# Kernel tuning notes

Hardware: AMD Instinct MI355X
Metric: run time of the kernel (lower is better)

## Reference

```python
import jax, jax.numpy as jnp
import numpy as np

B, S, D = 2, 2048, 2048
H = 16
KV_RANK = 512
NOPE, ROPE = 128, 64
QK_HD = NOPE + ROPE  # 192
V_HD = 128
SCALE = QK_HD ** -0.5
EPS = 1.1920929e-07  # torch RMSNorm default eps = finfo(fp32).eps
NEG = -1e9


def rmsnorm(x, w):
    return x * jax.lax.rsqrt(jnp.mean(x * x, axis=-1, keepdims=True) + EPS) * w


def apply_rope(x, freqs):
    # x: (b, s, h, r) interleaved pairs; freqs: (s, r//2) angles
    sh = x.shape
    xr = x.reshape(*sh[:-1], -1, 2)
    a, b = xr[..., 0], xr[..., 1]
    cos = jnp.cos(freqs)[None, :, None, :]
    sin = jnp.sin(freqs)[None, :, None, :]
    return jnp.stack([a * cos - b * sin, a * sin + b * cos], axis=-1).reshape(sh)


def setup_inputs() -> dict:
    key = jax.random.key(0)
    ks = jax.random.split(key, 8)
    inv = lambda k, shape, fan_in: jax.random.uniform(k, shape, jnp.float32, -1.0, 1.0) / np.sqrt(fan_in)
    x = jax.random.normal(ks[0], (B, S, D), jnp.float32)
    freqs = jax.random.uniform(ks[1], (S, ROPE // 2), jnp.float32) * np.float32(np.pi)
    mask = jnp.where(jnp.triu(jnp.ones((S, S), bool), k=1), jnp.float32(NEG), jnp.float32(0.0))
    wq_w = inv(ks[2], (H * QK_HD, D), D)
    wq_b = jnp.zeros((H * QK_HD,), jnp.float32)
    wkv_a_w = inv(ks[3], (KV_RANK + ROPE, D), D)
    wkv_a_b = jnp.zeros((KV_RANK + ROPE,), jnp.float32)
    kv_norm_w = jnp.ones((KV_RANK,), jnp.float32)
    wkv_b_w = inv(ks[4], (H * (NOPE + V_HD), KV_RANK), KV_RANK)
    wo_w = inv(ks[5], (D, H * V_HD), H * V_HD)
    wo_b = jnp.zeros((D,), jnp.float32)
    return dict(x=x, freqs=freqs, mask=mask, wq_w=wq_w, wq_b=wq_b,
                wkv_a_w=wkv_a_w, wkv_a_b=wkv_a_b, kv_norm_w=kv_norm_w,
                wkv_b_w=wkv_b_w, wo_w=wo_w, wo_b=wo_b)


def reference(x, freqs, mask, wq_w, wq_b, wkv_a_w, wkv_a_b, kv_norm_w, wkv_b_w, wo_w, wo_b):
    b, s, _ = x.shape
    # q projection (q_lora_rank == 0 path)
    q = (x @ wq_w.T + wq_b).reshape(b, s, H, QK_HD)
    q_nope, q_pe = q[..., :NOPE], q[..., NOPE:]
    q_pe = apply_rope(q_pe, freqs)
    # latent kv projection
    kv = x @ wkv_a_w.T + wkv_a_b
    kv, k_pe = kv[..., :KV_RANK], kv[..., KV_RANK:]
    k_pe = apply_rope(k_pe[:, :, None, :], freqs)[:, :, 0, :]  # (b, t, r)
    kv_proj = rmsnorm(kv, kv_norm_w)  # (b, t, c)
    wkv_b = wkv_b_w.reshape(H, NOPE + V_HD, KV_RANK)
    # absorb K-nope projection into q
    q_nope = jnp.einsum('bshd,hdc->bshc', q_nope, wkv_b[:, :NOPE])
    scores = (jnp.einsum('bshc,btc->bsht', q_nope, kv_proj)
              + jnp.einsum('bshr,btr->bsht', q_pe, k_pe)) * SCALE
    scores = scores + mask[None, :, None, :]
    scores = jax.nn.softmax(scores.astype(jnp.float32), axis=-1).astype(x.dtype)
    out = jnp.einsum('bsht,btc->bshc', scores, kv_proj)
    out = jnp.einsum('bshc,hdc->bshd', out, wkv_b[:, -V_HD:])
    return out.reshape(b, s, H * V_HD) @ wo_w.T + wo_b
```

## Files before the change

kernel.cpp:

```cpp
#include <hip/hip_runtime.h>
#include <hip/hip_bf16.h>
#include <math.h>

#define B_ 2
#define S_ 2048
#define H_ 16
#define SCALE_ 0.07216878364870323f
#define SL2_ (0.07216878364870323f * 1.4426950408889634f)
#define EPS_ 1.1920929e-07f
#define M0_ 8.0f

typedef __attribute__((ext_vector_type(8))) short bf16x8;
typedef __attribute__((ext_vector_type(4))) float f32x4;
union U4 { uint4 u; bf16x8 v; f32x4 f; };

__device__ __forceinline__ uint bfbits(float x) {
    uint u = __float_as_uint(x);
    return (u + 0x7fffu + ((u >> 16) & 1u)) >> 16;
}
__device__ __forceinline__ uint pack2bf(float a, float b) {
    return bfbits(a) | (bfbits(b) << 16);
}
__device__ __forceinline__ uint cvtpk(float a, float b) {
    uint r;
    asm("v_cvt_pk_bf16_f32 %0, %1, %2" : "=v"(r) : "v"(a), "v"(b));
    return r;
}
__device__ __forceinline__ void gld_lds16(const ushort* g, ushort* l) {
    __builtin_amdgcn_global_load_lds(
        (const __attribute__((address_space(1))) uint*)g,
        (__attribute__((address_space(3))) uint*)l, 16, 0, 0);
}

template<int OM>
__global__ __launch_bounds__(256) void mgemm(
    const ushort* __restrict__ A, int lda, long long aOff1, long long aOff2,
    const ushort* __restrict__ Bm, int ldb, long long bOff1, long long bOff2,
    const float* __restrict__ bias, float scale,
    void* __restrict__ Cv, int ldc, long long cOff1, long long cOff2,
    int K, int zDiv)
{
    __shared__ ushort As[128 * 32];
    __shared__ ushort Bs[128 * 32];

    const int z = blockIdx.z;
    const int z1 = z % zDiv, z2 = z / zDiv;
    A  += z1 * aOff1 + z2 * aOff2;
    Bm += z1 * bOff1 + z2 * bOff2;
    const long long cBase = z1 * cOff1 + z2 * cOff2;

    int bx = blockIdx.x, by = blockIdx.y;
    {
        const int gx = gridDim.x, total = gx * gridDim.y;
        if ((total & 7) == 0) {
            const int flat = bx + gx * by;
            const int nx = total >> 3;
            const int flat2 = (flat & 7) * nx + (flat >> 3);
            bx = flat2 % gx;
            by = flat2 / gx;
        }
    }
    const int n0 = bx * 128;
    const int m0 = by * 128;
    const int tid = threadIdx.x;
    const int w   = tid >> 6;
    const int l   = tid & 63;
    const int m   = l & 15;
    const int q4  = l >> 4;
    const int mw  = (w & 1) * 64;
    const int nw  = (w >> 1) * 64;
    const int sr  = l >> 2;
    const int sc  = l & 3;

    f32x4 acc[4][4];
#pragma unroll
    for (int i = 0; i < 4; ++i)
#pragma unroll
        for (int j = 0; j < 4; ++j) acc[i][j] = (f32x4){0.f, 0.f, 0.f, 0.f};

    for (int k0 = 0; k0 < K; k0 += 32) {
#pragma unroll
        for (int jj = 0; jj < 2; ++jj) {
            const int slot = w * 2 + jj;
            const int row  = slot * 16 + sr;
            const int g    = sc ^ ((row >> 1) & 3);
            gld_lds16(&A[(long long)(m0 + row) * lda + k0 + g * 8], &As[slot * 512]);
            gld_lds16(&Bm[(long long)(n0 + row) * ldb + k0 + g * 8], &Bs[slot * 512]);
        }
        __syncthreads();

        U4 af[4], bf[4];
#pragma unroll
        for (int i = 0; i < 4; ++i) {
            const int ra = mw + i * 16 + m;
            af[i].u = *(const uint4*)&As[ra * 32 + (q4 ^ ((ra >> 1) & 3)) * 8];
            const int rb = nw + i * 16 + m;
            bf[i].u = *(const uint4*)&Bs[rb * 32 + (q4 ^ ((rb >> 1) & 3)) * 8];
        }
#pragma unroll
        for (int i = 0; i < 4; ++i)
#pragma unroll
            for (int j = 0; j < 4; ++j)
                acc[i][j] = __builtin_amdgcn_mfma_f32_16x16x32_bf16(
                    af[i].v, bf[j].v, acc[i][j], 0, 0, 0);
        __syncthreads();
    }

#pragma unroll
    for (int j = 0; j < 4; ++j) {
        const int cn = n0 + nw + j * 16 + m;
        const float bv = bias ? bias[cn] : 0.0f;
#pragma unroll
        for (int i = 0; i < 4; ++i) {
            const int rw = m0 + mw + i * 16 + q4 * 4;
#pragma unroll
            for (int r = 0; r < 4; ++r) {
                const float val = acc[i][j][r] * scale + bv;
                if (OM == 0) {
                    ((float*)Cv)[cBase + (long long)(rw + r) * ldc + cn] = val;
                } else if (OM == 2) {
                    const int t = rw + r, d = cn;
                    const long long idx =
                        ((((long long)(z2 * 64 + (t >> 5)) * 16 + z1) * 8
                          + (d >> 5) * 2 + ((t >> 4) & 1)) * 64
                         + ((d >> 3) & 3) * 16 + (t & 15)) * 8 + (d & 7);
                    ((ushort*)Cv)[idx] = (ushort)bfbits(val);
                } else {
                    const int d = rw + r, t = cn;
                    const long long idx =
                        ((((long long)(z2 * 64 + (t >> 5)) * 16 + z1) * 8
                          + (d >> 4)) * 64
                         + ((t >> 3) & 3) * 16 + (d & 15)) * 8 + (t & 7);
                    ((ushort*)Cv)[idx] = (ushort)bfbits(val);
                }
            }
        }
    }
}

__global__ __launch_bounds__(256) void conv_all(
    const float* __restrict__ x, const float* __restrict__ wq,
    const float* __restrict__ wkva, const float* __restrict__ wo,
    const float* __restrict__ wkvb,
    ushort* __restrict__ x_bf, ushort* __restrict__ wq_bf,
    ushort* __restrict__ wkva_bf, ushort* __restrict__ wo_bf,
    ushort* __restrict__ wkvbK, ushort* __restrict__ wkvbV)
{
    const int bid = blockIdx.x;
    const int tid = threadIdx.x;
    if (bid < 8192) {
        const long long i = ((long long)bid * 256 + tid) * 4;
        float4 v = *(const float4*)&x[i];
        uint2 p; p.x = pack2bf(v.x, v.y); p.y = pack2bf(v.z, v.w);
        *(uint2*)&x_bf[i] = p;
    } else if (bid < 14336) {
        const long long i = ((long long)(bid - 8192) * 256 + tid) * 4;
        float4 v = *(const float4*)&wq[i];
        uint2 p; p.x = pack2bf(v.x, v.y); p.y = pack2bf(v.z, v.w);
        *(uint2*)&wq_bf[i] = p;
    } else if (bid < 15616) {
        const int i = ((bid - 14336) * 256 + tid) * 4;
        const int r = i >> 11;
        uint2 p = make_uint2(0u, 0u);
        if (r < 576) {
            float4 v = *(const float4*)&wkva[i];
            p.x = pack2bf(v.x, v.y); p.y = pack2bf(v.z, v.w);
        }
        *(uint2*)&wkva_bf[i] = p;
    } else if (bid < 19712) {
        const long long i = ((long long)(bid - 15616) * 256 + tid) * 4;
        float4 v = *(const float4*)&wo[i];
        uint2 p; p.x = pack2bf(v.x, v.y); p.y = pack2bf(v.z, v.w);
        *(uint2*)&wo_bf[i] = p;
    } else if (bid < 20736) {
        const int i = ((bid - 19712) * 256 + tid) * 4;
        const int h = i >> 16, rem = i & 65535;
        float4 v = *(const float4*)&wkvb[((long long)(h * 256)) * 512 + rem];
        uint2 p; p.x = pack2bf(v.x, v.y); p.y = pack2bf(v.z, v.w);
        *(uint2*)&wkvbK[i] = p;
    } else {
        const int i = ((bid - 20736) * 256 + tid) * 4;
        const int h = i >> 16, rem = i & 65535;
        float4 v = *(const float4*)&wkvb[((long long)(h * 256 + 128)) * 512 + rem];
        uint2 p; p.x = pack2bf(v.x, v.y); p.y = pack2bf(v.z, v.w);
        *(uint2*)&wkvbV[i] = p;
    }
}

__global__ __launch_bounds__(256) void qprep(
    const float* __restrict__ q_raw, const float* __restrict__ freqs,
    ushort* __restrict__ q192)
{
    const int idx = blockIdx.x * 256 + threadIdx.x;
    const int row = idx / 48;
    const int c4  = idx % 48;
    const int bs = row >> 4, h = row & 15;
    const float* src = q_raw + (long long)bs * 3072 + h * 192;
    if (c4 < 32) {
        const int d = c4 * 4;
        float4 v = *(const float4*)&src[d];
        uint2 p;
        p.x = pack2bf(v.x * SL2_, v.y * SL2_);
        p.y = pack2bf(v.z * SL2_, v.w * SL2_);
        *(uint2*)&q192[(long long)row * 192 + d] = p;
    } else {
        const int j = c4 - 32;
        const int s = bs & 2047;
        const float f0 = freqs[s * 32 + j * 2];
        const float f1 = freqs[s * 32 + j * 2 + 1];
        float c0, s0, c1, s1;
        __sincosf(f0, &s0, &c0);
        __sincosf(f1, &s1, &c1);
        float4 v = *(const float4*)&src[128 + j * 4];
        uint2 p;
        p.x = pack2bf((v.x * c0 - v.y * s0) * SL2_, (v.x * s0 + v.y * c0) * SL2_);
        p.y = pack2bf((v.z * c1 - v.w * s1) * SL2_, (v.z * s1 + v.w * c1) * SL2_);
        *(uint2*)&q192[(long long)row * 192 + 128 + j * 4] = p;
    }
}

__global__ __launch_bounds__(64) void kv_post_kernel(
    const float* __restrict__ kv_raw, const float* __restrict__ bias,
    const float* __restrict__ w, const float* __restrict__ freqs,
    ushort* __restrict__ kv_h, uint* __restrict__ rimg)
{
    const int bs = blockIdx.x;
    const int lane = threadIdx.x;
    const float* src = kv_raw + (long long)bs * 640;
    ushort* dst = kv_h + (long long)bs * 576;

    const int c = 4 * lane;
    float4 v0 = *(const float4*)&src[c];
    float4 v1 = *(const float4*)&src[256 + c];
    float4 b0 = *(const float4*)&bias[c];
    float4 b1 = *(const float4*)&bias[256 + c];
    v0.x += b0.x; v0.y += b0.y; v0.z += b0.z; v0.w += b0.w;
    v1.x += b1.x; v1.y += b1.y; v1.z += b1.z; v1.w += b1.w;
    float ss = v0.x * v0.x + v0.y * v0.y + v0.z * v0.z + v0.w * v0.w +
               v1.x * v1.x + v1.y * v1.y + v1.z * v1.z + v1.w * v1.w;
#pragma unroll
    for (int o = 32; o; o >>= 1) ss += __shfl_xor(ss, o, 64);
    const float rs = rsqrtf(ss * (1.0f / 512.0f) + EPS_);

    float4 w0 = *(const float4*)&w[c];
    float4 w1 = *(const float4*)&w[256 + c];
    uint2 p0, p1;
    p0.x = pack2bf(v0.x * rs * w0.x, v0.y * rs * w0.y);
    p0.y = pack2bf(v0.z * rs * w0.z, v0.w * rs * w0.w);
    p1.x = pack2bf(v1.x * rs * w1.x, v1.y * rs * w1.y);
    p1.y = pack2bf(v1.z * rs * w1.z, v1.w * rs * w1.w);
    *(uint2*)&dst[c] = p0;
    *(uint2*)&dst[256 + c] = p1;

    if (lane < 32) {
        const int b = bs >> 11, s = bs & 2047;
        const int j = lane;
        const float f = freqs[s * 32 + j];
        float cs, sn;
        __sincosf(f, &sn, &cs);
        const float a  = src[512 + 2 * j]     + bias[512 + 2 * j];
        const float b2 = src[512 + 2 * j + 1] + bias[512 + 2 * j + 1];
        const uint p = pack2bf(a * cs - b2 * sn, a * sn + b2 * cs);
        const long long idx =
            (((long long)(b * 64 + (s >> 5)) * 4 + (j >> 4) * 2 + ((s >> 4) & 1)) * 64
             + ((j >> 2) & 3) * 16 + (s & 15)) * 4 + (j & 3);
        rimg[idx] = p;
    }
}

__global__ __launch_bounds__(256, 2) void attn_kernel(
    const ushort* __restrict__ q192,
    const uint4*  __restrict__ khimg,
    const uint4*  __restrict__ rimg,
    const uint4*  __restrict__ vhimg,
    float* __restrict__ part_o,
    float* __restrict__ part_l)
{
    __shared__ uint buf[2][20 * 256];

    const int hb   = blockIdx.x;
    const int h    = hb & 15;
    const int b    = hb >> 4;
    const int p    = blockIdx.y;
    const int par  = blockIdx.z;
    const int tid  = threadIdx.x;
    const int wid  = tid >> 6;
    const int lane = tid & 63;
    const int m    = lane & 15;
    const int q4   = lane >> 4;
    const bool odd = q4 & 1;

    auto stage = [&](int bs, int it) {
        const long long tb = (long long)(b * 64 + it);
        const uint4* kb = khimg + ((tb * 16 + h) * 8) * 64;
        const uint4* rb = rimg  + (tb * 4) * 64;
        const uint4* vb = vhimg + ((tb * 16 + h) * 8) * 64;
        ushort* l = (ushort*)&buf[bs][0];
        gld_lds16((const ushort*)(kb + (wid    ) * 64 + lane), l + (wid     ) * 512);
        gld_lds16((const ushort*)(kb + (wid + 4) * 64 + lane), l + (wid +  4) * 512);
        gld_lds16((const ushort*)(rb + (wid    ) * 64 + lane), l + (wid +  8) * 512);
        gld_lds16((const ushort*)(vb + (wid    ) * 64 + lane), l + (wid + 12) * 512);
        gld_lds16((const ushort*)(vb + (wid + 4) * 64 + lane), l + (wid + 16) * 512);
    };

    int cur = 0;
    for (int pass = 0; pass < 2; ++pass) {
        const int chunk = pass ? p : (15 - p);
        const int row0a = chunk * 128 + wid * 16;
        const int row0b = row0a + 64;
        const int sRa   = row0a + m;
        const int sRb   = row0b + m;

        U4 qfa[6], qfb[6];
        {
            const uint4* qpa = (const uint4*)(q192 + ((long long)(b * S_ + sRa) * H_ + h) * 192);
            const uint4* qpb = (const uint4*)(q192 + ((long long)(b * S_ + sRb) * H_ + h) * 192);
#pragma unroll
            for (int f = 0; f < 6; ++f) { qfa[f].u = qpa[f * 4 + q4]; qfb[f].u = qpb[f * 4 + q4]; }
        }

        f32x4 oA[8], oB[8];
#pragma unroll
        for (int c = 0; c < 8; ++c) {
            oA[c] = (f32x4){0.f, 0.f, 0.f, 0.f};
            oB[c] = (f32x4){0.f, 0.f, 0.f, 0.f};
        }
        float lA = 0.0f, lB = 0.0f;

        auto softpack = [&](const f32x4 s0, const f32x4 s1, int t0v, int rw0,
                            float& lac) -> U4 {
            float p00, p01, p02, p03, p10, p11, p12, p13;
            if (t0v + 31 <= rw0) {
                p00 = exp2f(s0[0] - M0_); p01 = exp2f(s0[1] - M0_);
                p02 = exp2f(s0[2] - M0_); p03 = exp2f(s0[3] - M0_);
                p10 = exp2f(s1[0] - M0_); p11 = exp2f(s1[1] - M0_);
                p12 = exp2f(s1[2] - M0_); p13 = exp2f(s1[3] - M0_);
            } else {
                const int sR = rw0 + m;
                const int tb0 = t0v + q4 * 4;
                const int tb1 = tb0 + 16;
                p00 = (tb0 + 0 <= sR) ? exp2f(s0[0] - M0_) : 0.0f;
                p01 = (tb0 + 1 <= sR) ? exp2f(s0[1] - M0_) : 0.0f;
                p02 = (tb0 + 2 <= sR) ? exp2f(s0[2] - M0_) : 0.0f;
                p03 = (tb0 + 3 <= sR) ? exp2f(s0[3] - M0_) : 0.0f;
                p10 = (tb1 + 0 <= sR) ? exp2f(s1[0] - M0_) : 0.0f;
                p11 = (tb1 + 1 <= sR) ? exp2f(s1[1] - M0_) : 0.0f;
                p12 = (tb1 + 2 <= sR) ? exp2f(s1[2] - M0_) : 0.0f;
                p13 = (tb1 + 3 <= sR) ? exp2f(s1[3] - M0_) : 0.0f;
            }
            lac += (p00 + p01) + (p02 + p03) + (p10 + p11) + (p12 + p13);
            uint X0 = cvtpk(p00, p01), X1 = cvtpk(p02, p03);
            uint Y0 = cvtpk(p10, p11), Y1 = cvtpk(p12, p13);
            asm("v_permlane32_swap_b32 %0, %1" : "+v"(X0), "+v"(Y0));
            asm("v_permlane32_swap_b32 %0, %1" : "+v"(X1), "+v"(Y1));
            uint u0 = odd ? X0 : Y0;
            uint u1 = odd ? X1 : Y1;
            uint w0 = (uint)__builtin_amdgcn_ds_swizzle((int)u0, 0x401F);
            uint w1 = (uint)__builtin_amdgcn_ds_swizzle((int)u1, 0x401F);
            U4 bb;
            bb.u.x = odd ? w0 : X0;
            bb.u.y = odd ? w1 : X1;
            bb.u.z = odd ? Y0 : w0;
            bb.u.w = odd ? Y1 : w1;
            return bb;
        };

        const int nT2 = 2 * chunk + 2;
        __syncthreads();
        stage(cur, par);

        for (int v = 0; v < nT2; ++v) {
            const int it = 2 * v + par;
            const int t0 = it * 32;
            __syncthreads();
            if (v + 1 < nT2) stage(cur ^ 1, it + 2);
            __builtin_amdgcn_sched_barrier(0);

            const uint* bb0 = &buf[cur][0];
            const int abase = lane * 4;
            const bool liveB = (t0 <= row0b + 15);
            const bool liveA = (t0 <= row0a + 15);
            const bool twoA  = (t0 < row0a);
            const bool twoB  = (t0 < row0b);

            if (liveB) {
                f32x4 sA0 = (f32x4){0.f,0.f,0.f,0.f}, sA1 = (f32x4){0.f,0.f,0.f,0.f};
                f32x4 sB0 = (f32x4){0.f,0.f,0.f,0.f}, sB1 = (f32x4){0.f,0.f,0.f,0.f};

                if (twoA) {
#pragma unroll
                    for (int f = 0; f < 6; ++f) {
                        const int ck = (f < 4) ? f * 2 : (f - 4) * 2 + 8;
                        U4 a0, a1;
                        a0.u = *(const uint4*)&bb0[ck * 256 + abase];
                        a1.u = *(const uint4*)&bb0[(ck + 1) * 256 + abase];
                        sA0 = __builtin_amdgcn_mfma_f32_16x16x32_bf16(a0.v, qfa[f].v, sA0, 0, 0, 0);
                        sB0 = __builtin_amdgcn_mfma_f32_16x16x32_bf16(a0.v, qfb[f].v, sB0, 0, 0, 0);
                        sA1 = __builtin_amdgcn_mfma_f32_16x16x32_bf16(a1.v, qfa[f].v, sA1, 0, 0, 0);
                        sB1 = __builtin_amdgcn_mfma_f32_16x16x32_bf16(a1.v, qfb[f].v, sB1, 0, 0, 0);
                    }
                } else {
#pragma unroll
                    for (int f = 0; f < 6; ++f) {
                        const int ck = (f < 4) ? f * 2 : (f - 4) * 2 + 8;
                        U4 a0;
                        a0.u = *(const uint4*)&bb0[ck * 256 + abase];
                        if (liveA)
                            sA0 = __builtin_amdgcn_mfma_f32_16x16x32_bf16(a0.v, qfa[f].v, sA0, 0, 0, 0);
                        sB0 = __builtin_amdgcn_mfma_f32_16x16x32_bf16(a0.v, qfb[f].v, sB0, 0, 0, 0);
                        if (twoB) {
                            U4 a1;
                            a1.u = *(const uint4*)&bb0[(ck + 1) * 256 + abase];
                            sB1 = __builtin_amdgcn_mfma_f32_16x16x32_bf16(a1.v, qfb[f].v, sB1, 0, 0, 0);
                        }
                    }
                }

                U4 bbB = softpack(sB0, sB1, t0, row0b, lB);
                if (liveA) {
                    U4 bbA = softpack(sA0, sA1, t0, row0a, lA);
#pragma unroll
                    for (int c = 0; c < 8; ++c) {
                        U4 av; av.u = *(const uint4*)&bb0[(12 + c) * 256 + abase];
                        oB[c] = __builtin_amdgcn_mfma_f32_16x16x32_bf16(av.v, bbB.v, oB[c], 0, 0, 0);
                        oA[c] = __builtin_amdgcn_mfma_f32_16x16x32_bf16(av.v, bbA.v, oA[c], 0, 0, 0);
                    }
                } else {
#pragma unroll
                    for (int c = 0; c < 8; ++c) {
                        U4 av; av.u = *(const uint4*)&bb0[(12 + c) * 256 + abase];
                        oB[c] = __builtin_amdgcn_mfma_f32_16x16x32_bf16(av.v, bbB.v, oB[c], 0, 0, 0);
                    }
                }
            }
            cur ^= 1;
        }

        lA += __shfl_xor(lA, 16, 64);
        lA += __shfl_xor(lA, 32, 64);
        lB += __shfl_xor(lB, 16, 64);
        lB += __shfl_xor(lB, 32, 64);

        const int cid  = (b * 16 + h) * 16 + chunk;
        const int slot = cid * 2 + par;
        float* po = part_o + (long long)slot * 16384;
        const int rA = wid * 16 + m;
        const int rB = rA + 64;
#pragma unroll
        for (int c = 0; c < 8; ++c) {
            *(f32x4*)&po[rA * 128 + c * 16 + q4 * 4] = oA[c];
            *(f32x4*)&po[rB * 128 + c * 16 + q4 * 4] = oB[c];
        }
        if (q4 == 0) {
            part_l[slot * 128 + rA] = lA;
            part_l[slot * 128 + rB] = lB;
        }
    }
}

__global__ __launch_bounds__(256) void combine_kernel(
    const float* __restrict__ part_o, const float* __restrict__ part_l,
    ushort* __restrict__ o_h)
{
    const int idx = blockIdx.x * 256 + threadIdx.x;
    const int d4  = (idx & 31) * 4;
    const int r   = (idx >> 5) & 127;
    const int cid = idx >> 12;
    const int chunk = cid & 15, h = (cid >> 4) & 15, b = cid >> 8;
    const long long s0 = (long long)(cid * 2) * 16384 + r * 128 + d4;
    float4 a = *(const float4*)&part_o[s0];
    float4 c = *(const float4*)&part_o[s0 + 16384];
    const float l = part_l[cid * 256 + r] + part_l[cid * 256 + 128 + r];
    const float inv = 1.0f / l;
    uint2 pk;
    pk.x = cvtpk((a.x + c.x) * inv, (a.y + c.y) * inv);
    pk.y = cvtpk((a.z + c.z) * inv, (a.w + c.w) * inv);
    const int s = chunk * 128 + r;
    *(uint2*)&o_h[(((long long)(b * S_ + s)) * H_ + h) * 128 + d4] = pk;
}

extern "C" void kernel_launch(void* const* d_in, const int* in_sizes, int n_in,
                              void* d_out, int out_size, void* d_ws, size_t ws_size,
                              hipStream_t stream)
{
    const float* x         = (const float*)d_in[0];
    const float* freqs     = (const float*)d_in[1];
    const float* wq_w      = (const float*)d_in[3];
    const float* wq_b      = (const float*)d_in[4];
    const float* wkv_a_w   = (const float*)d_in[5];
    const float* wkv_a_b   = (const float*)d_in[6];
    const float* kv_norm_w = (const float*)d_in[7];
    const float* wkv_b_w   = (const float*)d_in[8];
    const float* wo_w      = (const float*)d_in[9];
    const float* wo_b      = (const float*)d_in[10];
    float* out = (float*)d_out;

    char* w = (char*)d_ws;
    ushort* wo_bf   = (ushort*)w;  w += 8388608;
    uint4*  khimg   = (uint4*)w;   w += 16777216;
    uint4*  vhimg   = (uint4*)w;   w += 16777216;
    uint4*  rimg    = (uint4*)w;   w += 524288;
    ushort* q192    = (ushort*)w;  w += 25165824;
    ushort* o_h     = (ushort*)w;  w += 16777216;
    char* SCR = w;
    ushort* x_bf    = (ushort*)(SCR);
    ushort* wq_bf   = (ushort*)(SCR + 16777216);
    ushort* wkva_bf = (ushort*)(SCR + 29360128);
    ushort* wkvbK   = (ushort*)(SCR + 31981568);
    ushort* wkvbV   = (ushort*)(SCR + 34078720);
    float*  kv_raw  = (float*)(SCR + 36175872);
    float*  q_raw   = (float*)(SCR + 46661632);
    ushort* kv_h    = (ushort*)(SCR);
    float*  part_o  = (float*)(SCR);
    float*  part_l  = (float*)(SCR + 67108864);

    dim3 blk(256);

    conv_all<<<dim3(21760), blk, 0, stream>>>(
        x, wq_w, wkv_a_w, wo_w, wkv_b_w,
        x_bf, wq_bf, wkva_bf, wo_bf, wkvbK, wkvbV);

    mgemm<0><<<dim3(24, 32, 1), blk, 0, stream>>>(
        x_bf, 2048, 0LL, 0LL, wq_bf, 2048, 0LL, 0LL, wq_b, 1.0f,
        q_raw, 3072, 0LL, 0LL, 2048, 1);

    mgemm<0><<<dim3(5, 32, 1), blk, 0, stream>>>(
        x_bf, 2048, 0LL, 0LL, wkva_bf, 2048, 0LL, 0LL, nullptr, 1.0f,
        kv_raw, 640, 0LL, 0LL, 2048, 1);

    qprep<<<dim3(12288), blk, 0, stream>>>(q_raw, freqs, q192);

    kv_post_kernel<<<dim3(4096), dim3(64), 0, stream>>>(
        kv_raw, wkv_a_b, kv_norm_w, freqs, kv_h, (uint*)rimg);

    mgemm<2><<<dim3(1, 16, 32), blk, 0, stream>>>(
        kv_h, 576, 0LL, (long long)S_ * 576,
        wkvbK, 512, 65536LL, 0LL, nullptr, 1.0f,
        khimg, 0, 0LL, 0LL, 512, 16);
    mgemm<3><<<dim3(16, 1, 32), blk, 0, stream>>>(
        wkvbV, 512, 65536LL, 0LL,
        kv_h, 576, 0LL, (long long)S_ * 576, nullptr, 1.0f,
        vhimg, 0, 0LL, 0LL, 512, 16);

    attn_kernel<<<dim3(32, 8, 2), blk, 0, stream>>>(
        q192, khimg, rimg, vhimg, part_o, part_l);

    combine_kernel<<<dim3(8192), blk, 0, stream>>>(part_o, part_l, o_h);

    mgemm<0><<<dim3(16, 32, 1), blk, 0, stream>>>(
        o_h, 2048, 0LL, 0LL, wo_bf, 2048, 0LL, 0LL, wo_b, 1.0f,
        out, 2048, 0LL, 0LL, 2048, 1);
}
```

Measured before the change: 443.6 us.

## Double-buffer GEMM LDS tiles and fuse q RoPE/scale/bf16 epilogue into Q GEMM

The shared GEMM kernel now uses two LDS buffers, prefetching the next K-tile while MFMAs run on the current one, and drops one barrier per iteration. A new epilogue mode in the Q projection GEMM applies bias, RoPE (pairing lanes with a shuffle and computing sincos), the softmax scale and bf16 conversion directly. This removes the separate qprep kernel and the fp32 q_raw round-trip through memory. The cost is doubled LDS use per block and sincos work repeated in the GEMM epilogue.

```diff
diff --git a/kernel.cpp b/kernel.cpp
--- a/kernel.cpp
+++ b/kernel.cpp
@@ -38,10 +38,10 @@
     const ushort* __restrict__ Bm, int ldb, long long bOff1, long long bOff2,
     const float* __restrict__ bias, float scale,
     void* __restrict__ Cv, int ldc, long long cOff1, long long cOff2,
-    int K, int zDiv)
+    int K, int zDiv, const float* __restrict__ freqs)
 {
-    __shared__ ushort As[128 * 32];
-    __shared__ ushort Bs[128 * 32];
+    __shared__ ushort As[2][128 * 32];
+    __shared__ ushort Bs[2][128 * 32];
 
     const int z = blockIdx.z;
     const int z1 = z % zDiv, z2 = z / zDiv;
@@ -72,30 +72,37 @@
     const int sr  = l >> 2;
     const int sc  = l & 3;
 
-    f32x4 acc[4][4];
-#pragma unroll
-    for (int i = 0; i < 4; ++i)
-#pragma unroll
-        for (int j = 0; j < 4; ++j) acc[i][j] = (f32x4){0.f, 0.f, 0.f, 0.f};
-
-    for (int k0 = 0; k0 < K; k0 += 32) {
+    auto stageT = [&](int bi, int k0) {
 #pragma unroll
         for (int jj = 0; jj < 2; ++jj) {
             const int slot = w * 2 + jj;
             const int row  = slot * 16 + sr;
             const int g    = sc ^ ((row >> 1) & 3);
-            gld_lds16(&A[(long long)(m0 + row) * lda + k0 + g * 8], &As[slot * 512]);
-            gld_lds16(&Bm[(long long)(n0 + row) * ldb + k0 + g * 8], &Bs[slot * 512]);
-        }
+            gld_lds16(&A[(long long)(m0 + row) * lda + k0 + g * 8], &As[bi][slot * 512]);
+            gld_lds16(&Bm[(long long)(n0 + row) * ldb + k0 + g * 8], &Bs[bi][slot * 512]);
+        }
+    };
+
+    f32x4 acc[4][4];
+#pragma unroll
+    for (int i = 0; i < 4; ++i)
+#pragma unroll
+        for (int j = 0; j < 4; ++j) acc[i][j] = (f32x4){0.f, 0.f, 0.f, 0.f};
+
+    stageT(0, 0);
+    int cur = 0;
+    for (int k0 = 0; k0 < K; k0 += 32) {
         __syncthreads();
+        if (k0 + 32 < K) stageT(cur ^ 1, k0 + 32);
+        __builtin_amdgcn_sched_barrier(0);
 
         U4 af[4], bf[4];
 #pragma unroll
         for (int i = 0; i < 4; ++i) {
             const int ra = mw + i * 16 + m;
-            af[i].u = *(const uint4*)&As[ra * 32 + (q4 ^ ((ra >> 1) & 3)) * 8];
+            af[i].u = *(const uint4*)&As[cur][ra * 32 + (q4 ^ ((ra >> 1) & 3)) * 8];
             const int rb = nw + i * 16 + m;
-            bf[i].u = *(const uint4*)&Bs[rb * 32 + (q4 ^ ((rb >> 1) & 3)) * 8];
+            bf[i].u = *(const uint4*)&Bs[cur][rb * 32 + (q4 ^ ((rb >> 1) & 3)) * 8];
         }
 #pragma unroll
         for (int i = 0; i < 4; ++i)
@@ -103,22 +110,40 @@
             for (int j = 0; j < 4; ++j)
                 acc[i][j] = __builtin_amdgcn_mfma_f32_16x16x32_bf16(
                     af[i].v, bf[j].v, acc[i][j], 0, 0, 0);
-        __syncthreads();
+        cur ^= 1;
     }
 
 #pragma unroll
     for (int j = 0; j < 4; ++j) {
         const int cn = n0 + nw + j * 16 + m;
         const float bv = bias ? bias[cn] : 0.0f;
-#pragma unroll
-        for (int i = 0; i < 4; ++i) {
-            const int rw = m0 + mw + i * 16 + q4 * 4;
+        const int d192 = cn % 192;
+        const bool ropeW = (OM == 1) && (d192 >= 128);
+        const int ri = (d192 - 128) >> 1;
+        const bool evn = !(cn & 1);
+#pragma unroll
+        for (int i2 = 0; i2 < 4; ++i2) {
+            const int rw = m0 + mw + i2 * 16 + q4 * 4;
 #pragma unroll
             for (int r = 0; r < 4; ++r) {
-                const float val = acc[i][j][r] * scale + bv;
                 if (OM == 0) {
+                    const float val = acc[i2][j][r] * scale + bv;
                     ((float*)Cv)[cBase + (long long)(rw + r) * ldc + cn] = val;
+                } else if (OM == 1) {
+                    float val = acc[i2][j][r] + bv;
+                    if (ropeW) {
+                        const float pv = __shfl_xor(val, 1, 64);
+                        const float a  = evn ? val : pv;
+                        const float b  = evn ? pv : val;
+                        const int s = (rw + r) & 2047;
+                        float cs, sn;
+                        __sincosf(freqs[s * 32 + ri], &sn, &cs);
+                        val = evn ? (a * cs - b * sn) : (a * sn + b * cs);
+                    }
+                    ((ushort*)Cv)[cBase + (long long)(rw + r) * ldc + cn] =
+                        (ushort)bfbits(val * SL2_);
                 } else if (OM == 2) {
+                    const float val = acc[i2][j][r] * scale + bv;
                     const int t = rw + r, d = cn;
                     const long long idx =
                         ((((long long)(z2 * 64 + (t >> 5)) * 16 + z1) * 8
@@ -126,6 +151,7 @@
                          + ((d >> 3) & 3) * 16 + (t & 15)) * 8 + (d & 7);
                     ((ushort*)Cv)[idx] = (ushort)bfbits(val);
                 } else {
+                    const float val = acc[i2][j][r] * scale + bv;
                     const int d = rw + r, t = cn;
                     const long long idx =
                         ((((long long)(z2 * 64 + (t >> 5)) * 16 + z1) * 8
@@ -184,38 +210,6 @@
         float4 v = *(const float4*)&wkvb[((long long)(h * 256 + 128)) * 512 + rem];
         uint2 p; p.x = pack2bf(v.x, v.y); p.y = pack2bf(v.z, v.w);
         *(uint2*)&wkvbV[i] = p;
-    }
-}
-
-__global__ __launch_bounds__(256) void qprep(
-    const float* __restrict__ q_raw, const float* __restrict__ freqs,
-    ushort* __restrict__ q192)
-{
-    const int idx = blockIdx.x * 256 + threadIdx.x;
-    const int row = idx / 48;
-    const int c4  = idx % 48;
-    const int bs = row >> 4, h = row & 15;
-    const float* src = q_raw + (long long)bs * 3072 + h * 192;
-    if (c4 < 32) {
-        const int d = c4 * 4;
-        float4 v = *(const float4*)&src[d];
-        uint2 p;
-        p.x = pack2bf(v.x * SL2_, v.y * SL2_);
-        p.y = pack2bf(v.z * SL2_, v.w * SL2_);
-        *(uint2*)&q192[(long long)row * 192 + d] = p;
-    } else {
-        const int j = c4 - 32;
-        const int s = bs & 2047;
-        const float f0 = freqs[s * 32 + j * 2];
-        const float f1 = freqs[s * 32 + j * 2 + 1];
-        float c0, s0, c1, s1;
-        __sincosf(f0, &s0, &c0);
-        __sincosf(f1, &s1, &c1);
-        float4 v = *(const float4*)&src[128 + j * 4];
-        uint2 p;
-        p.x = pack2bf((v.x * c0 - v.y * s0) * SL2_, (v.x * s0 + v.y * c0) * SL2_);
-        p.y = pack2bf((v.z * c1 - v.w * s1) * SL2_, (v.z * s1 + v.w * c1) * SL2_);
-        *(uint2*)&q192[(long long)row * 192 + 128 + j * 4] = p;
     }
 }
 
@@ -509,7 +503,6 @@
     ushort* wkvbK   = (ushort*)(SCR + 31981568);
     ushort* wkvbV   = (ushort*)(SCR + 34078720);
     float*  kv_raw  = (float*)(SCR + 36175872);
-    float*  q_raw   = (float*)(SCR + 46661632);
     ushort* kv_h    = (ushort*)(SCR);
     float*  part_o  = (float*)(SCR);
     float*  part_l  = (float*)(SCR + 67108864);
@@ -520,15 +513,13 @@
         x, wq_w, wkv_a_w, wo_w, wkv_b_w,
         x_bf, wq_bf, wkva_bf, wo_bf, wkvbK, wkvbV);
 
-    mgemm<0><<<dim3(24, 32, 1), blk, 0, stream>>>(
+    mgemm<1><<<dim3(24, 32, 1), blk, 0, stream>>>(
         x_bf, 2048, 0LL, 0LL, wq_bf, 2048, 0LL, 0LL, wq_b, 1.0f,
-        q_raw, 3072, 0LL, 0LL, 2048, 1);
+        q192, 3072, 0LL, 0LL, 2048, 1, freqs);
 
     mgemm<0><<<dim3(5, 32, 1), blk, 0, stream>>>(
         x_bf, 2048, 0LL, 0LL, wkva_bf, 2048, 0LL, 0LL, nullptr, 1.0f,
-        kv_raw, 640, 0LL, 0LL, 2048, 1);
-
-    qprep<<<dim3(12288), blk, 0, stream>>>(q_raw, freqs, q192);
+        kv_raw, 640, 0LL, 0LL, 2048, 1, nullptr);
 
     kv_post_kernel<<<dim3(4096), dim3(64), 0, stream>>>(
         kv_raw, wkv_a_b, kv_norm_w, freqs, kv_h, (uint*)rimg);
@@ -536,11 +527,11 @@
     mgemm<2><<<dim3(1, 16, 32), blk, 0, stream>>>(
         kv_h, 576, 0LL, (long long)S_ * 576,
         wkvbK, 512, 65536LL, 0LL, nullptr, 1.0f,
-        khimg, 0, 0LL, 0LL, 512, 16);
+        khimg, 0, 0LL, 0LL, 512, 16, nullptr);
     mgemm<3><<<dim3(16, 1, 32), blk, 0, stream>>>(
         wkvbV, 512, 65536LL, 0LL,
         kv_h, 576, 0LL, (long long)S_ * 576, nullptr, 1.0f,
-        vhimg, 0, 0LL, 0LL, 512, 16);
+        vhimg, 0, 0LL, 0LL, 512, 16, nullptr);
 
     attn_kernel<<<dim3(32, 8, 2), blk, 0, stream>>>(
         q192, khimg, rimg, vhimg, part_o, part_l);
@@ -549,5 +540,5 @@
 
     mgemm<0><<<dim3(16, 32, 1), blk, 0, stream>>>(
         o_h, 2048, 0LL, 0LL, wo_bf, 2048, 0LL, 0LL, wo_b, 1.0f,
-        out, 2048, 0LL, 0LL, 2048, 1);
-}
+        out, 2048, 0LL, 0LL, 2048, 1, nullptr);
+}
```

New measurement: 440.2 us. About the same (-0.8%).
